# Kernel tuning notes

Hardware: AMD Instinct MI355X
Metric: run time of the kernel (lower is better)

The kernel has to match this reference:

```python
import jax, jax.numpy as jnp
import numpy as np

WINDOW_SIZE = 11
SIGMA = 1.5
C1 = 0.01 ** 2
C2 = 0.03 ** 2
MSE_WEIGHT = 1.0
SSIM_WEIGHT = 0.01


def _gaussian_window(channels):
    # 1D gaussian, normalized, then outer product -> [C,1,K,K] depthwise kernel
    coords = np.arange(WINDOW_SIZE) - WINDOW_SIZE // 2
    g = np.exp(-(coords ** 2) / (2.0 * SIGMA ** 2))
    g = g / g.sum()
    w2d = np.outer(g, g).astype(np.float32)  # [K,K]
    w = np.tile(w2d[None, None], (channels, 1, 1, 1))  # [C,1,K,K]
    return jnp.asarray(w)


def _depthwise_conv(x, w):
    # x: [B,C,H,W], w: [C,1,K,K]; SAME padding, groups=C (matches torch conv2d pad=K//2, groups=C)
    pad = WINDOW_SIZE // 2
    return jax.lax.conv_general_dilated(
        x, w,
        window_strides=(1, 1),
        padding=[(pad, pad), (pad, pad)],
        dimension_numbers=('NCHW', 'OIHW', 'NCHW'),
        feature_group_count=x.shape[1],
    )


def setup_inputs() -> dict:
    key = jax.random.key(0)
    k1, k2 = jax.random.split(key)
    shape = (32, 3, 512, 512)
    predicted = jax.random.uniform(k1, shape, dtype=jnp.float32)
    target = jax.random.uniform(k2, shape, dtype=jnp.float32)
    return {"predicted": predicted, "target": target}


def reference(predicted, target):
    # MSE part
    mse_l = jnp.mean((predicted - target) ** 2)

    # SSIM part (standard pytorch-ssim: gaussian window, size_average=True)
    C = predicted.shape[1]
    w = _gaussian_window(C)

    mu1 = _depthwise_conv(predicted, w)
    mu2 = _depthwise_conv(target, w)
    mu1_sq = mu1 * mu1
    mu2_sq = mu2 * mu2
    mu1_mu2 = mu1 * mu2

    sigma1_sq = _depthwise_conv(predicted * predicted, w) - mu1_sq
    sigma2_sq = _depthwise_conv(target * target, w) - mu2_sq
    sigma12 = _depthwise_conv(predicted * target, w) - mu1_mu2

    ssim_map = ((2.0 * mu1_mu2 + C1) * (2.0 * sigma12 + C2)) / (
        (mu1_sq + mu2_sq + C1) * (sigma1_sq + sigma2_sq + C2)
    )
    ssim_val = jnp.mean(ssim_map)

    return MSE_WEIGHT * mse_l + SSIM_WEIGHT * (1.0 - ssim_val)
```

## Files before the change

kernel.cpp:

```cpp
#include <hip/hip_runtime.h>
#include <hip/hip_fp16.h>


#define WSZ   512
#define TW    64
#define TH    32
#define HALO  5
#define IN_H  (TH + 2*HALO)
#define NPOS  32
#define GX    (WSZ / TW)
#define GY    (WSZ / TH)
#define NSLOT 64
#define SSIM_C1 0.0001f
#define SSIM_C2 0.0009f

#define W0 0.00102838f
#define W1 0.00759876f
#define W2 0.03600080f
#define W3 0.10936080f
#define W4 0.21300560f
#define W5 0.26601170f

static __device__ __forceinline__ __half2 pk(float a, float b) {
    return __builtin_bit_cast(__half2, __builtin_amdgcn_cvt_pkrtz(a, b));
}
static __device__ __forceinline__ __half2 stagger(__half2 hi, __half2 lo) {
    return __builtin_bit_cast(__half2,
        __builtin_amdgcn_alignbit(__builtin_bit_cast(unsigned, hi),
                                  __builtin_bit_cast(unsigned, lo), 16));
}

__launch_bounds__(256, 6)
__global__ void fused_mse_ssim(const float* __restrict__ P,
                               const float* __restrict__ T,
                               float* __restrict__ ws) {
    __shared__ float4 sAB[IN_H][NPOS];
    __shared__ float  red[2][4];

    const int tid = threadIdx.x;
    const int gx0 = blockIdx.x * TW;
    const int gy0 = blockIdx.y * TH;
    const size_t plane = (size_t)blockIdx.z * (WSZ * (size_t)WSZ);
    const float* Pp = P + plane;
    const float* Tp = T + plane;

    const float gwf[11] = {W0,W1,W2,W3,W4,W5,W4,W3,W2,W1,W0};
    unsigned gwh[11];
    #pragma unroll
    for (int k = 0; k < 11; ++k)
        gwh[k] = __builtin_amdgcn_readfirstlane(
                     __builtin_bit_cast(unsigned, __float2half2_rn(gwf[k])));

    float mse = 0.f;

    const bool interior = (blockIdx.x != 0) && (blockIdx.x != GX - 1) &&
                          (blockIdx.y != 0) && (blockIdx.y != GY - 1);

    for (int it = tid; it < IN_H * 8; it += 256) {
        const int r  = it >> 3;
        const int q  = it & 7;
        const int gy = gy0 - HALO + r;
        const int cb = gx0 + q * 8 - 8;
        const float* prow = Pp + ((long)gy * WSZ + cb);
        const float* trow = Tp + ((long)gy * WSZ + cb);
        const bool mrow = ((unsigned)(r - HALO) < (unsigned)TH);

        __half2 As[12], Ad[12];

        if (interior) {
            #pragma unroll
            for (int b = 0; b < 6; ++b) {
                const float4 pv = *(const float4*)(prow + 4 * b);
                const float4 tv = *(const float4*)(trow + 4 * b);
                const float s0 = pv.x + tv.x, s1 = pv.y + tv.y;
                const float s2 = pv.z + tv.z, s3 = pv.w + tv.w;
                const float d0 = pv.x - tv.x, d1 = pv.y - tv.y;
                const float d2 = pv.z - tv.z, d3 = pv.w - tv.w;
                As[2*b]   = pk(s0, s1); As[2*b+1] = pk(s2, s3);
                Ad[2*b]   = pk(d0, d1); Ad[2*b+1] = pk(d2, d3);
                if ((b == 2 || b == 3) && mrow) {
                    mse = fmaf(d0, d0, mse); mse = fmaf(d1, d1, mse);
                    mse = fmaf(d2, d2, mse); mse = fmaf(d3, d3, mse);
                }
            }
        } else {
            const bool rv = ((unsigned)gy < (unsigned)WSZ);
            #pragma unroll
            for (int b = 0; b < 6; ++b) {
                const unsigned c = (unsigned)(cb + 4 * b);
                float4 pv = make_float4(0.f, 0.f, 0.f, 0.f);
                float4 tv = make_float4(0.f, 0.f, 0.f, 0.f);
                if (rv && c < (unsigned)WSZ) {
                    pv = *(const float4*)(prow + 4 * b);
                    tv = *(const float4*)(trow + 4 * b);
                }
                const float s0 = pv.x + tv.x, s1 = pv.y + tv.y;
                const float s2 = pv.z + tv.z, s3 = pv.w + tv.w;
                const float d0 = pv.x - tv.x, d1 = pv.y - tv.y;
                const float d2 = pv.z - tv.z, d3 = pv.w - tv.w;
                As[2*b]   = pk(s0, s1); As[2*b+1] = pk(s2, s3);
                Ad[2*b]   = pk(d0, d1); Ad[2*b+1] = pk(d2, d3);
                if ((b == 2 || b == 3) && mrow) {
                    mse = fmaf(d0, d0, mse); mse = fmaf(d1, d1, mse);
                    mse = fmaf(d2, d2, mse); mse = fmaf(d3, d3, mse);
                }
            }
        }

        const __half2 z = __float2half2_rn(0.f);
        __half2 aS[4]  = {z, z, z, z};
        __half2 aD[4]  = {z, z, z, z};
        __half2 aSS[4] = {z, z, z, z};
        __half2 aDD[4] = {z, z, z, z};

        #pragma unroll
        for (int jj = 0; jj <= 16; ++jj) {
            const int j = jj + 3;
            __half2 vs, vd;
            if (j & 1) {
                vs = stagger(As[(j >> 1) + 1], As[j >> 1]);
                vd = stagger(Ad[(j >> 1) + 1], Ad[j >> 1]);
            } else {
                vs = As[j >> 1];
                vd = Ad[j >> 1];
            }
            const __half2 vss = __hmul2(vs, vs);
            const __half2 vdd = __hmul2(vd, vd);
            #pragma unroll
            for (int m = 0; m < 4; ++m) {
                const int k = jj - 2 * m;
                if (k >= 0 && k < 11) {
                    const __half2 w = __builtin_bit_cast(__half2, gwh[k]);
                    aS[m]  = __hfma2(w, vs,  aS[m]);
                    aD[m]  = __hfma2(w, vd,  aD[m]);
                    aSS[m] = __hfma2(w, vss, aSS[m]);
                    aDD[m] = __hfma2(w, vdd, aDD[m]);
                }
            }
        }

        #pragma unroll
        for (int m = 0; m < 4; ++m)
            sAB[r][8 * m + q] = make_float4(
                __builtin_bit_cast(float, aS[m]),  __builtin_bit_cast(float, aD[m]),
                __builtin_bit_cast(float, aSS[m]), __builtin_bit_cast(float, aDD[m]));
    }
    __syncthreads();

    const int q2  = tid & 31;
    const int col = ((q2 & 3) << 3) | (q2 >> 2);
    const int y0  = (tid >> 5) << 2;

    const __half2 z2 = __float2half2_rn(0.f);
    __half2 acc[4][4];
    #pragma unroll
    for (int a = 0; a < 4; ++a) {
        acc[a][0] = z2; acc[a][1] = z2; acc[a][2] = z2; acc[a][3] = z2;
    }

    #pragma unroll
    for (int j = 0; j < 14; ++j) {
        const float4 ab = sAB[y0 + j][col];
        const __half2 hS  = __builtin_bit_cast(__half2, ab.x);
        const __half2 hD  = __builtin_bit_cast(__half2, ab.y);
        const __half2 hSS = __builtin_bit_cast(__half2, ab.z);
        const __half2 hDD = __builtin_bit_cast(__half2, ab.w);
        #pragma unroll
        for (int a = 0; a < 4; ++a) {
            const int k = j - a;
            if (k >= 0 && k < 11) {
                const __half2 w = __builtin_bit_cast(__half2, gwh[k]);
                acc[a][0] = __hfma2(w, hS,  acc[a][0]);
                acc[a][1] = __hfma2(w, hD,  acc[a][1]);
                acc[a][2] = __hfma2(w, hSS, acc[a][2]);
                acc[a][3] = __hfma2(w, hDD, acc[a][3]);
            }
        }
    }

    float ssim = 0.f;
    #pragma unroll
    for (int a = 0; a < 4; ++a) {
        const float2 Av = __half22float2(acc[a][0]);
        const float2 Bv = __half22float2(acc[a][1]);
        const float2 Xv = __half22float2(acc[a][2]);
        const float2 Yv = __half22float2(acc[a][3]);
        #pragma unroll
        for (int e = 0; e < 2; ++e) {
            const float A = e ? Av.y : Av.x;
            const float B = e ? Bv.y : Bv.x;
            const float X = e ? Xv.y : Xv.x;
            const float Y = e ? Yv.y : Yv.x;
            const float a2 = A * A;
            const float b2 = B * B;
            const float P1 = a2 + b2;
            const float M1 = a2 - b2;
            const float num1 = fmaf(0.5f, M1, SSIM_C1);
            const float den1 = fmaf(0.5f, P1, SSIM_C1);
            const float num2 = fmaf(0.5f, (X - Y) - M1, SSIM_C2);
            const float den2 = fmaf(0.5f, (X + Y) - P1, SSIM_C2);
            ssim = fmaf(num1 * num2, __builtin_amdgcn_rcpf(den1 * den2), ssim);
        }
    }

    #pragma unroll
    for (int off = 32; off > 0; off >>= 1) {
        mse  += __shfl_down(mse, off);
        ssim += __shfl_down(ssim, off);
    }
    const int wid = tid >> 6;
    if ((tid & 63) == 0) { red[0][wid] = mse; red[1][wid] = ssim; }
    __syncthreads();
    if (tid == 0) {
        const float m = red[0][0] + red[0][1] + red[0][2] + red[0][3];
        const float s = red[1][0] + red[1][1] + red[1][2] + red[1][3];
        const int bid  = (blockIdx.z * gridDim.y + blockIdx.y) * gridDim.x + blockIdx.x;
        const int slot = (bid & (NSLOT - 1)) * 16;
        atomicAdd(&ws[slot + 0], m);
        atomicAdd(&ws[slot + 1], s);
    }
}

__global__ void finalize_loss(const float* __restrict__ ws,
                              float* __restrict__ out, float invN) {
    const int t = threadIdx.x;
    float m = ws[t * 16 + 0];
    float s = ws[t * 16 + 1];
    #pragma unroll
    for (int off = 32; off > 0; off >>= 1) {
        m += __shfl_down(m, off);
        s += __shfl_down(s, off);
    }
    if (t == 0) out[0] = m * invN + 0.01f * (1.f - s * invN);
}

extern "C" void kernel_launch(void* const* d_in, const int* in_sizes, int n_in,
                              void* d_out, int out_size, void* d_ws, size_t ws_size,
                              hipStream_t stream) {
    const float* P = (const float*)d_in[0];
    const float* T = (const float*)d_in[1];
    float* out = (float*)d_out;
    float* ws  = (float*)d_ws;

    const int planes = in_sizes[0] / (WSZ * WSZ);
    const float invN = 1.f / (float)in_sizes[0];

    (void)hipMemsetAsync(ws, 0, NSLOT * 16 * sizeof(float), stream);
    dim3 grid(GX, GY, planes);
    fused_mse_ssim<<<grid, 256, 0, stream>>>(P, T, ws);
    finalize_loss<<<1, 64, 0, stream>>>(ws, out, invN);
}
```

Baseline: 234.3 us.

## Stream row chunks through a ring buffer per block and fuse finalize via last-block reduction

Each block now covers a 64x256 strip and walks it in 32-row chunks, keeping horizontally blurred rows in a 48-row circular shared buffer. Only the first chunk loads the 10-row halo, so redundant halo loads and the horizontal pass on them are removed. The separate finalize kernel is replaced by a last-block-done atomic counter that performs the final reduction inside the main kernel, saving a launch. The cost is a smaller grid with fewer, longer blocks, which lowers parallelism and latency hiding, plus an extra barrier per chunk.

```diff
diff --git a/kernel.cpp b/kernel.cpp
--- a/kernel.cpp
+++ b/kernel.cpp
@@ -4,12 +4,13 @@
 
 #define WSZ   512
 #define TW    64
-#define TH    32
+#define GX    (WSZ / TW)
+#define HH    256
+#define CH    32
+#define NCH   (HH / CH)
+#define BUF   48
+#define NPOS  32
 #define HALO  5
-#define IN_H  (TH + 2*HALO)
-#define NPOS  32
-#define GX    (WSZ / TW)
-#define GY    (WSZ / TH)
 #define NSLOT 64
 #define SSIM_C1 0.0001f
 #define SSIM_C2 0.0009f
@@ -33,16 +34,20 @@
 __launch_bounds__(256, 6)
 __global__ void fused_mse_ssim(const float* __restrict__ P,
                                const float* __restrict__ T,
-                               float* __restrict__ ws) {
-    __shared__ float4 sAB[IN_H][NPOS];
+                               float* __restrict__ ws,
+                               float* __restrict__ out,
+                               float invN, int nblocks) {
+    __shared__ float4 sAB[BUF][NPOS];
     __shared__ float  red[2][4];
+    __shared__ int    sLast;
 
     const int tid = threadIdx.x;
     const int gx0 = blockIdx.x * TW;
-    const int gy0 = blockIdx.y * TH;
+    const int gyb = blockIdx.y * HH;
     const size_t plane = (size_t)blockIdx.z * (WSZ * (size_t)WSZ);
     const float* Pp = P + plane;
     const float* Tp = T + plane;
+    const bool xedge = (blockIdx.x == 0) || (blockIdx.x == GX - 1);
 
     const float gwf[11] = {W0,W1,W2,W3,W4,W5,W4,W3,W2,W1,W0};
     unsigned gwh[11];
@@ -52,155 +57,168 @@
                      __builtin_bit_cast(unsigned, __float2half2_rn(gwf[k])));
 
     float mse = 0.f;
-
-    const bool interior = (blockIdx.x != 0) && (blockIdx.x != GX - 1) &&
-                          (blockIdx.y != 0) && (blockIdx.y != GY - 1);
-
-    for (int it = tid; it < IN_H * 8; it += 256) {
-        const int r  = it >> 3;
-        const int q  = it & 7;
-        const int gy = gy0 - HALO + r;
-        const int cb = gx0 + q * 8 - 8;
-        const float* prow = Pp + ((long)gy * WSZ + cb);
-        const float* trow = Tp + ((long)gy * WSZ + cb);
-        const bool mrow = ((unsigned)(r - HALO) < (unsigned)TH);
-
-        __half2 As[12], Ad[12];
-
-        if (interior) {
-            #pragma unroll
-            for (int b = 0; b < 6; ++b) {
-                const float4 pv = *(const float4*)(prow + 4 * b);
-                const float4 tv = *(const float4*)(trow + 4 * b);
-                const float s0 = pv.x + tv.x, s1 = pv.y + tv.y;
-                const float s2 = pv.z + tv.z, s3 = pv.w + tv.w;
-                const float d0 = pv.x - tv.x, d1 = pv.y - tv.y;
-                const float d2 = pv.z - tv.z, d3 = pv.w - tv.w;
-                As[2*b]   = pk(s0, s1); As[2*b+1] = pk(s2, s3);
-                Ad[2*b]   = pk(d0, d1); Ad[2*b+1] = pk(d2, d3);
-                if ((b == 2 || b == 3) && mrow) {
-                    mse = fmaf(d0, d0, mse); mse = fmaf(d1, d1, mse);
-                    mse = fmaf(d2, d2, mse); mse = fmaf(d3, d3, mse);
-                }
-            }
-        } else {
-            const bool rv = ((unsigned)gy < (unsigned)WSZ);
-            #pragma unroll
-            for (int b = 0; b < 6; ++b) {
-                const unsigned c = (unsigned)(cb + 4 * b);
-                float4 pv = make_float4(0.f, 0.f, 0.f, 0.f);
-                float4 tv = make_float4(0.f, 0.f, 0.f, 0.f);
-                if (rv && c < (unsigned)WSZ) {
-                    pv = *(const float4*)(prow + 4 * b);
-                    tv = *(const float4*)(trow + 4 * b);
-                }
-                const float s0 = pv.x + tv.x, s1 = pv.y + tv.y;
-                const float s2 = pv.z + tv.z, s3 = pv.w + tv.w;
-                const float d0 = pv.x - tv.x, d1 = pv.y - tv.y;
-                const float d2 = pv.z - tv.z, d3 = pv.w - tv.w;
-                As[2*b]   = pk(s0, s1); As[2*b+1] = pk(s2, s3);
-                Ad[2*b]   = pk(d0, d1); Ad[2*b+1] = pk(d2, d3);
-                if ((b == 2 || b == 3) && mrow) {
-                    mse = fmaf(d0, d0, mse); mse = fmaf(d1, d1, mse);
-                    mse = fmaf(d2, d2, mse); mse = fmaf(d3, d3, mse);
-                }
-            }
+    float ssim = 0.f;
+
+    for (int c = 0; c < NCH; ++c) {
+        const int nIt = (c == 0) ? 42 * 8 : 32 * 8;
+        const int lrb = (c == 0) ? 0 : c * CH + 2 * HALO;
+        for (int it = tid; it < nIt; it += 256) {
+            const int r    = it >> 3;
+            const int q    = it & 7;
+            const int lr   = lrb + r;
+            const int gy   = gyb + lr - HALO;
+            const int slot = lr % BUF;
+            const bool rv   = ((unsigned)gy < (unsigned)WSZ);
+            const bool mrow = ((unsigned)(lr - HALO) < (unsigned)HH);
+            const int cb = gx0 + q * 8 - 8;
+            const float* prow = Pp + ((long)gy * WSZ + cb);
+            const float* trow = Tp + ((long)gy * WSZ + cb);
+
+            const __half2 z = __float2half2_rn(0.f);
+            __half2 As[12], Ad[12];
+
+            if (!xedge) {
+                if (rv) {
+                    #pragma unroll
+                    for (int b = 0; b < 6; ++b) {
+                        const float4 pv = *(const float4*)(prow + 4 * b);
+                        const float4 tv = *(const float4*)(trow + 4 * b);
+                        const float s0 = pv.x + tv.x, s1 = pv.y + tv.y;
+                        const float s2 = pv.z + tv.z, s3 = pv.w + tv.w;
+                        const float d0 = pv.x - tv.x, d1 = pv.y - tv.y;
+                        const float d2 = pv.z - tv.z, d3 = pv.w - tv.w;
+                        As[2*b]   = pk(s0, s1); As[2*b+1] = pk(s2, s3);
+                        Ad[2*b]   = pk(d0, d1); Ad[2*b+1] = pk(d2, d3);
+                        if ((b == 2 || b == 3) && mrow) {
+                            mse = fmaf(d0, d0, mse); mse = fmaf(d1, d1, mse);
+                            mse = fmaf(d2, d2, mse); mse = fmaf(d3, d3, mse);
+                        }
+                    }
+                } else {
+                    #pragma unroll
+                    for (int b = 0; b < 12; ++b) { As[b] = z; Ad[b] = z; }
+                }
+            } else {
+                #pragma unroll
+                for (int b = 0; b < 6; ++b) {
+                    const unsigned cc = (unsigned)(cb + 4 * b);
+                    float4 pv = make_float4(0.f, 0.f, 0.f, 0.f);
+                    float4 tv = make_float4(0.f, 0.f, 0.f, 0.f);
+                    if (rv && cc < (unsigned)WSZ) {
+                        pv = *(const float4*)(prow + 4 * b);
+                        tv = *(const float4*)(trow + 4 * b);
+                    }
+                    const float s0 = pv.x + tv.x, s1 = pv.y + tv.y;
+                    const float s2 = pv.z + tv.z, s3 = pv.w + tv.w;
+                    const float d0 = pv.x - tv.x, d1 = pv.y - tv.y;
+                    const float d2 = pv.z - tv.z, d3 = pv.w - tv.w;
+                    As[2*b]   = pk(s0, s1); As[2*b+1] = pk(s2, s3);
+                    Ad[2*b]   = pk(d0, d1); Ad[2*b+1] = pk(d2, d3);
+                    if ((b == 2 || b == 3) && mrow) {
+                        mse = fmaf(d0, d0, mse); mse = fmaf(d1, d1, mse);
+                        mse = fmaf(d2, d2, mse); mse = fmaf(d3, d3, mse);
+                    }
+                }
+            }
+
+            __half2 aS[4]  = {z, z, z, z};
+            __half2 aD[4]  = {z, z, z, z};
+            __half2 aSS[4] = {z, z, z, z};
+            __half2 aDD[4] = {z, z, z, z};
+
+            #pragma unroll
+            for (int jj = 0; jj <= 16; ++jj) {
+                const int j = jj + 3;
+                __half2 vs, vd;
+                if (j & 1) {
+                    vs = stagger(As[(j >> 1) + 1], As[j >> 1]);
+                    vd = stagger(Ad[(j >> 1) + 1], Ad[j >> 1]);
+                } else {
+                    vs = As[j >> 1];
+                    vd = Ad[j >> 1];
+                }
+                const __half2 vss = __hmul2(vs, vs);
+                const __half2 vdd = __hmul2(vd, vd);
+                #pragma unroll
+                for (int m = 0; m < 4; ++m) {
+                    const int k = jj - 2 * m;
+                    if (k >= 0 && k < 11) {
+                        const __half2 w = __builtin_bit_cast(__half2, gwh[k]);
+                        aS[m]  = __hfma2(w, vs,  aS[m]);
+                        aD[m]  = __hfma2(w, vd,  aD[m]);
+                        aSS[m] = __hfma2(w, vss, aSS[m]);
+                        aDD[m] = __hfma2(w, vdd, aDD[m]);
+                    }
+                }
+            }
+
+            #pragma unroll
+            for (int m = 0; m < 4; ++m)
+                sAB[slot][8 * m + q] = make_float4(
+                    __builtin_bit_cast(float, aS[m]),  __builtin_bit_cast(float, aD[m]),
+                    __builtin_bit_cast(float, aSS[m]), __builtin_bit_cast(float, aDD[m]));
         }
-
-        const __half2 z = __float2half2_rn(0.f);
-        __half2 aS[4]  = {z, z, z, z};
-        __half2 aD[4]  = {z, z, z, z};
-        __half2 aSS[4] = {z, z, z, z};
-        __half2 aDD[4] = {z, z, z, z};
-
-        #pragma unroll
-        for (int jj = 0; jj <= 16; ++jj) {
-            const int j = jj + 3;
-            __half2 vs, vd;
-            if (j & 1) {
-                vs = stagger(As[(j >> 1) + 1], As[j >> 1]);
-                vd = stagger(Ad[(j >> 1) + 1], Ad[j >> 1]);
-            } else {
-                vs = As[j >> 1];
-                vd = Ad[j >> 1];
-            }
-            const __half2 vss = __hmul2(vs, vs);
-            const __half2 vdd = __hmul2(vd, vd);
-            #pragma unroll
-            for (int m = 0; m < 4; ++m) {
-                const int k = jj - 2 * m;
-                if (k >= 0 && k < 11) {
-                    const __half2 w = __builtin_bit_cast(__half2, gwh[k]);
-                    aS[m]  = __hfma2(w, vs,  aS[m]);
-                    aD[m]  = __hfma2(w, vd,  aD[m]);
-                    aSS[m] = __hfma2(w, vss, aSS[m]);
-                    aDD[m] = __hfma2(w, vdd, aDD[m]);
+        __syncthreads();
+
+        {
+            const int q2  = tid & 31;
+            const int col = ((q2 & 3) << 3) | (q2 >> 2);
+            const int y0l = c * CH + ((tid >> 5) << 2);
+            const int s0  = y0l % BUF;
+
+            const __half2 z2 = __float2half2_rn(0.f);
+            __half2 acc[4][4];
+            #pragma unroll
+            for (int a = 0; a < 4; ++a) {
+                acc[a][0] = z2; acc[a][1] = z2; acc[a][2] = z2; acc[a][3] = z2;
+            }
+
+            #pragma unroll
+            for (int j = 0; j < 14; ++j) {
+                int s = s0 + j; if (s >= BUF) s -= BUF;
+                const float4 ab = sAB[s][col];
+                const __half2 hS  = __builtin_bit_cast(__half2, ab.x);
+                const __half2 hD  = __builtin_bit_cast(__half2, ab.y);
+                const __half2 hSS = __builtin_bit_cast(__half2, ab.z);
+                const __half2 hDD = __builtin_bit_cast(__half2, ab.w);
+                #pragma unroll
+                for (int a = 0; a < 4; ++a) {
+                    const int k = j - a;
+                    if (k >= 0 && k < 11) {
+                        const __half2 w = __builtin_bit_cast(__half2, gwh[k]);
+                        acc[a][0] = __hfma2(w, hS,  acc[a][0]);
+                        acc[a][1] = __hfma2(w, hD,  acc[a][1]);
+                        acc[a][2] = __hfma2(w, hSS, acc[a][2]);
+                        acc[a][3] = __hfma2(w, hDD, acc[a][3]);
+                    }
+                }
+            }
+
+            #pragma unroll
+            for (int a = 0; a < 4; ++a) {
+                const float2 Av = __half22float2(acc[a][0]);
+                const float2 Bv = __half22float2(acc[a][1]);
+                const float2 Xv = __half22float2(acc[a][2]);
+                const float2 Yv = __half22float2(acc[a][3]);
+                #pragma unroll
+                for (int e = 0; e < 2; ++e) {
+                    const float A = e ? Av.y : Av.x;
+                    const float B = e ? Bv.y : Bv.x;
+                    const float X = e ? Xv.y : Xv.x;
+                    const float Y = e ? Yv.y : Yv.x;
+                    const float a2 = A * A;
+                    const float b2 = B * B;
+                    const float P1 = a2 + b2;
+                    const float M1 = a2 - b2;
+                    const float num1 = fmaf(0.5f, M1, SSIM_C1);
+                    const float den1 = fmaf(0.5f, P1, SSIM_C1);
+                    const float num2 = fmaf(0.5f, (X - Y) - M1, SSIM_C2);
+                    const float den2 = fmaf(0.5f, (X + Y) - P1, SSIM_C2);
+                    ssim = fmaf(num1 * num2, __builtin_amdgcn_rcpf(den1 * den2), ssim);
                 }
             }
         }
-
-        #pragma unroll
-        for (int m = 0; m < 4; ++m)
-            sAB[r][8 * m + q] = make_float4(
-                __builtin_bit_cast(float, aS[m]),  __builtin_bit_cast(float, aD[m]),
-                __builtin_bit_cast(float, aSS[m]), __builtin_bit_cast(float, aDD[m]));
-    }
-    __syncthreads();
-
-    const int q2  = tid & 31;
-    const int col = ((q2 & 3) << 3) | (q2 >> 2);
-    const int y0  = (tid >> 5) << 2;
-
-    const __half2 z2 = __float2half2_rn(0.f);
-    __half2 acc[4][4];
-    #pragma unroll
-    for (int a = 0; a < 4; ++a) {
-        acc[a][0] = z2; acc[a][1] = z2; acc[a][2] = z2; acc[a][3] = z2;
-    }
-
-    #pragma unroll
-    for (int j = 0; j < 14; ++j) {
-        const float4 ab = sAB[y0 + j][col];
-        const __half2 hS  = __builtin_bit_cast(__half2, ab.x);
-        const __half2 hD  = __builtin_bit_cast(__half2, ab.y);
-        const __half2 hSS = __builtin_bit_cast(__half2, ab.z);
-        const __half2 hDD = __builtin_bit_cast(__half2, ab.w);
-        #pragma unroll
-        for (int a = 0; a < 4; ++a) {
-            const int k = j - a;
-            if (k >= 0 && k < 11) {
-                const __half2 w = __builtin_bit_cast(__half2, gwh[k]);
-                acc[a][0] = __hfma2(w, hS,  acc[a][0]);
-                acc[a][1] = __hfma2(w, hD,  acc[a][1]);
-                acc[a][2] = __hfma2(w, hSS, acc[a][2]);
-                acc[a][3] = __hfma2(w, hDD, acc[a][3]);
-            }
-        }
-    }
-
-    float ssim = 0.f;
-    #pragma unroll
-    for (int a = 0; a < 4; ++a) {
-        const float2 Av = __half22float2(acc[a][0]);
-        const float2 Bv = __half22float2(acc[a][1]);
-        const float2 Xv = __half22float2(acc[a][2]);
-        const float2 Yv = __half22float2(acc[a][3]);
-        #pragma unroll
-        for (int e = 0; e < 2; ++e) {
-            const float A = e ? Av.y : Av.x;
-            const float B = e ? Bv.y : Bv.x;
-            const float X = e ? Xv.y : Xv.x;
-            const float Y = e ? Yv.y : Yv.x;
-            const float a2 = A * A;
-            const float b2 = B * B;
-            const float P1 = a2 + b2;
-            const float M1 = a2 - b2;
-            const float num1 = fmaf(0.5f, M1, SSIM_C1);
-            const float den1 = fmaf(0.5f, P1, SSIM_C1);
-            const float num2 = fmaf(0.5f, (X - Y) - M1, SSIM_C2);
-            const float den2 = fmaf(0.5f, (X + Y) - P1, SSIM_C2);
-            ssim = fmaf(num1 * num2, __builtin_amdgcn_rcpf(den1 * den2), ssim);
-        }
+        __syncthreads();
     }
 
     #pragma unroll
@@ -218,20 +236,25 @@
         const int slot = (bid & (NSLOT - 1)) * 16;
         atomicAdd(&ws[slot + 0], m);
         atomicAdd(&ws[slot + 1], s);
-    }
-}
-
-__global__ void finalize_loss(const float* __restrict__ ws,
-                              float* __restrict__ out, float invN) {
-    const int t = threadIdx.x;
-    float m = ws[t * 16 + 0];
-    float s = ws[t * 16 + 1];
-    #pragma unroll
-    for (int off = 32; off > 0; off >>= 1) {
-        m += __shfl_down(m, off);
-        s += __shfl_down(s, off);
-    }
-    if (t == 0) out[0] = m * invN + 0.01f * (1.f - s * invN);
+        __threadfence();
+        const unsigned old = __hip_atomic_fetch_add(
+            (unsigned*)(ws + NSLOT * 16), 1u,
+            __ATOMIC_ACQ_REL, __HIP_MEMORY_SCOPE_AGENT);
+        sLast = (old == (unsigned)(nblocks - 1)) ? 1 : 0;
+    }
+    __syncthreads();
+    if (sLast && tid < 64) {
+        float m = __hip_atomic_load(&ws[tid * 16 + 0], __ATOMIC_ACQUIRE,
+                                    __HIP_MEMORY_SCOPE_AGENT);
+        float s = __hip_atomic_load(&ws[tid * 16 + 1], __ATOMIC_ACQUIRE,
+                                    __HIP_MEMORY_SCOPE_AGENT);
+        #pragma unroll
+        for (int off = 32; off > 0; off >>= 1) {
+            m += __shfl_down(m, off);
+            s += __shfl_down(s, off);
+        }
+        if (tid == 0) out[0] = m * invN + 0.01f * (1.f - s * invN);
+    }
 }
 
 extern "C" void kernel_launch(void* const* d_in, const int* in_sizes, int n_in,
@@ -242,11 +265,11 @@
     float* out = (float*)d_out;
     float* ws  = (float*)d_ws;
 
-    const int planes = in_sizes[0] / (WSZ * WSZ);
-    const float invN = 1.f / (float)in_sizes[0];
-
-    (void)hipMemsetAsync(ws, 0, NSLOT * 16 * sizeof(float), stream);
-    dim3 grid(GX, GY, planes);
-    fused_mse_ssim<<<grid, 256, 0, stream>>>(P, T, ws);
-    finalize_loss<<<1, 64, 0, stream>>>(ws, out, invN);
-}
+    const int planes  = in_sizes[0] / (WSZ * WSZ);
+    const float invN  = 1.f / (float)in_sizes[0];
+    const int nblocks = GX * 2 * planes;
+
+    (void)hipMemsetAsync(ws, 0, (NSLOT * 16 + 16) * sizeof(float), stream);
+    dim3 grid(GX, 2, planes);
+    fused_mse_ssim<<<grid, 256, 0, stream>>>(P, T, ws, out, invN, nblocks);
+}
```

Measured after the change: 374.8 us. 60.0% more time.

## Use taller 64x64 tiles with 640 threads and swizzled shared layout

Applied to the files above, without the earlier changes.

Doubles tile height to 64 rows so the 10-row halo is amortized over more output rows, which cuts redundant horizontal-pass work and global reads. The block grows to 640 threads so each thread handles exactly one horizontal-pass row segment; 512 of them then run the vertical pass and 128 sit idle. The shared-memory column index is rotated by row to spread LDS bank accesses, and edge handling now keys on the x edge only, with row validity checked per thread. The larger block and the 8-blocks-per-CU launch bound raise register pressure and leave some threads idle.

```diff
diff --git a/kernel.cpp b/kernel.cpp
--- a/kernel.cpp
+++ b/kernel.cpp
@@ -4,12 +4,12 @@
 
 #define WSZ   512
 #define TW    64
-#define TH    32
+#define TH    64
 #define HALO  5
 #define IN_H  (TH + 2*HALO)
-#define NPOS  32
 #define GX    (WSZ / TW)
 #define GY    (WSZ / TH)
+#define NTHR  640
 #define NSLOT 64
 #define SSIM_C1 0.0001f
 #define SSIM_C2 0.0009f
@@ -30,12 +30,12 @@
                                   __builtin_bit_cast(unsigned, lo), 16));
 }
 
-__launch_bounds__(256, 6)
+__launch_bounds__(NTHR, 8)
 __global__ void fused_mse_ssim(const float* __restrict__ P,
                                const float* __restrict__ T,
                                float* __restrict__ ws) {
-    __shared__ float4 sAB[IN_H][NPOS];
-    __shared__ float  red[2][4];
+    __shared__ float4 sAB[IN_H][32];
+    __shared__ float  red[2][NTHR / 64];
 
     const int tid = threadIdx.x;
     const int gx0 = blockIdx.x * TW;
@@ -43,6 +43,7 @@
     const size_t plane = (size_t)blockIdx.z * (WSZ * (size_t)WSZ);
     const float* Pp = P + plane;
     const float* Tp = T + plane;
+    const bool xedge = (blockIdx.x == 0) || (blockIdx.x == GX - 1);
 
     const float gwf[11] = {W0,W1,W2,W3,W4,W5,W4,W3,W2,W1,W0};
     unsigned gwh[11];
@@ -53,25 +54,50 @@
 
     float mse = 0.f;
 
-    const bool interior = (blockIdx.x != 0) && (blockIdx.x != GX - 1) &&
-                          (blockIdx.y != 0) && (blockIdx.y != GY - 1);
-
-    for (int it = tid; it < IN_H * 8; it += 256) {
-        const int r  = it >> 3;
-        const int q  = it & 7;
+    if (tid < IN_H * 8) {
+        const int r  = tid >> 3;
+        const int g  = tid & 7;
         const int gy = gy0 - HALO + r;
-        const int cb = gx0 + q * 8 - 8;
+        const int cb = gx0 + g * 8 - 8;
         const float* prow = Pp + ((long)gy * WSZ + cb);
         const float* trow = Tp + ((long)gy * WSZ + cb);
+        const bool rv   = ((unsigned)gy < (unsigned)WSZ);
         const bool mrow = ((unsigned)(r - HALO) < (unsigned)TH);
 
+        const __half2 z = __float2half2_rn(0.f);
         __half2 As[12], Ad[12];
 
-        if (interior) {
+        if (!xedge) {
+            if (rv) {
+                #pragma unroll
+                for (int b = 0; b < 6; ++b) {
+                    const float4 pv = *(const float4*)(prow + 4 * b);
+                    const float4 tv = *(const float4*)(trow + 4 * b);
+                    const float s0 = pv.x + tv.x, s1 = pv.y + tv.y;
+                    const float s2 = pv.z + tv.z, s3 = pv.w + tv.w;
+                    const float d0 = pv.x - tv.x, d1 = pv.y - tv.y;
+                    const float d2 = pv.z - tv.z, d3 = pv.w - tv.w;
+                    As[2*b]   = pk(s0, s1); As[2*b+1] = pk(s2, s3);
+                    Ad[2*b]   = pk(d0, d1); Ad[2*b+1] = pk(d2, d3);
+                    if ((b == 2 || b == 3) && mrow) {
+                        mse = fmaf(d0, d0, mse); mse = fmaf(d1, d1, mse);
+                        mse = fmaf(d2, d2, mse); mse = fmaf(d3, d3, mse);
+                    }
+                }
+            } else {
+                #pragma unroll
+                for (int b = 0; b < 12; ++b) { As[b] = z; Ad[b] = z; }
+            }
+        } else {
             #pragma unroll
             for (int b = 0; b < 6; ++b) {
-                const float4 pv = *(const float4*)(prow + 4 * b);
-                const float4 tv = *(const float4*)(trow + 4 * b);
+                const unsigned cc = (unsigned)(cb + 4 * b);
+                float4 pv = make_float4(0.f, 0.f, 0.f, 0.f);
+                float4 tv = make_float4(0.f, 0.f, 0.f, 0.f);
+                if (rv && cc < (unsigned)WSZ) {
+                    pv = *(const float4*)(prow + 4 * b);
+                    tv = *(const float4*)(trow + 4 * b);
+                }
                 const float s0 = pv.x + tv.x, s1 = pv.y + tv.y;
                 const float s2 = pv.z + tv.z, s3 = pv.w + tv.w;
                 const float d0 = pv.x - tv.x, d1 = pv.y - tv.y;
@@ -83,31 +109,8 @@
                     mse = fmaf(d2, d2, mse); mse = fmaf(d3, d3, mse);
                 }
             }
-        } else {
-            const bool rv = ((unsigned)gy < (unsigned)WSZ);
-            #pragma unroll
-            for (int b = 0; b < 6; ++b) {
-                const unsigned c = (unsigned)(cb + 4 * b);
-                float4 pv = make_float4(0.f, 0.f, 0.f, 0.f);
-                float4 tv = make_float4(0.f, 0.f, 0.f, 0.f);
-                if (rv && c < (unsigned)WSZ) {
-                    pv = *(const float4*)(prow + 4 * b);
-                    tv = *(const float4*)(trow + 4 * b);
-                }
-                const float s0 = pv.x + tv.x, s1 = pv.y + tv.y;
-                const float s2 = pv.z + tv.z, s3 = pv.w + tv.w;
-                const float d0 = pv.x - tv.x, d1 = pv.y - tv.y;
-                const float d2 = pv.z - tv.z, d3 = pv.w - tv.w;
-                As[2*b]   = pk(s0, s1); As[2*b+1] = pk(s2, s3);
-                Ad[2*b]   = pk(d0, d1); Ad[2*b+1] = pk(d2, d3);
-                if ((b == 2 || b == 3) && mrow) {
-                    mse = fmaf(d0, d0, mse); mse = fmaf(d1, d1, mse);
-                    mse = fmaf(d2, d2, mse); mse = fmaf(d3, d3, mse);
-                }
-            }
-        }
-
-        const __half2 z = __float2half2_rn(0.f);
+        }
+
         __half2 aS[4]  = {z, z, z, z};
         __half2 aD[4]  = {z, z, z, z};
         __half2 aSS[4] = {z, z, z, z};
@@ -141,65 +144,68 @@
 
         #pragma unroll
         for (int m = 0; m < 4; ++m)
-            sAB[r][8 * m + q] = make_float4(
+            sAB[r][(4 * g + m + r) & 31] = make_float4(
                 __builtin_bit_cast(float, aS[m]),  __builtin_bit_cast(float, aD[m]),
                 __builtin_bit_cast(float, aSS[m]), __builtin_bit_cast(float, aDD[m]));
     }
     __syncthreads();
 
-    const int q2  = tid & 31;
-    const int col = ((q2 & 3) << 3) | (q2 >> 2);
-    const int y0  = (tid >> 5) << 2;
-
-    const __half2 z2 = __float2half2_rn(0.f);
-    __half2 acc[4][4];
-    #pragma unroll
-    for (int a = 0; a < 4; ++a) {
-        acc[a][0] = z2; acc[a][1] = z2; acc[a][2] = z2; acc[a][3] = z2;
-    }
-
-    #pragma unroll
-    for (int j = 0; j < 14; ++j) {
-        const float4 ab = sAB[y0 + j][col];
-        const __half2 hS  = __builtin_bit_cast(__half2, ab.x);
-        const __half2 hD  = __builtin_bit_cast(__half2, ab.y);
-        const __half2 hSS = __builtin_bit_cast(__half2, ab.z);
-        const __half2 hDD = __builtin_bit_cast(__half2, ab.w);
+    float ssim = 0.f;
+
+    if (tid < 512) {
+        const int q2 = tid & 31;
+        const int y0 = (tid >> 5) << 2;
+
+        const __half2 z2 = __float2half2_rn(0.f);
+        __half2 acc[4][4];
         #pragma unroll
         for (int a = 0; a < 4; ++a) {
-            const int k = j - a;
-            if (k >= 0 && k < 11) {
-                const __half2 w = __builtin_bit_cast(__half2, gwh[k]);
-                acc[a][0] = __hfma2(w, hS,  acc[a][0]);
-                acc[a][1] = __hfma2(w, hD,  acc[a][1]);
-                acc[a][2] = __hfma2(w, hSS, acc[a][2]);
-                acc[a][3] = __hfma2(w, hDD, acc[a][3]);
-            }
-        }
-    }
-
-    float ssim = 0.f;
-    #pragma unroll
-    for (int a = 0; a < 4; ++a) {
-        const float2 Av = __half22float2(acc[a][0]);
-        const float2 Bv = __half22float2(acc[a][1]);
-        const float2 Xv = __half22float2(acc[a][2]);
-        const float2 Yv = __half22float2(acc[a][3]);
-        #pragma unroll
-        for (int e = 0; e < 2; ++e) {
-            const float A = e ? Av.y : Av.x;
-            const float B = e ? Bv.y : Bv.x;
-            const float X = e ? Xv.y : Xv.x;
-            const float Y = e ? Yv.y : Yv.x;
-            const float a2 = A * A;
-            const float b2 = B * B;
-            const float P1 = a2 + b2;
-            const float M1 = a2 - b2;
-            const float num1 = fmaf(0.5f, M1, SSIM_C1);
-            const float den1 = fmaf(0.5f, P1, SSIM_C1);
-            const float num2 = fmaf(0.5f, (X - Y) - M1, SSIM_C2);
-            const float den2 = fmaf(0.5f, (X + Y) - P1, SSIM_C2);
-            ssim = fmaf(num1 * num2, __builtin_amdgcn_rcpf(den1 * den2), ssim);
+            acc[a][0] = z2; acc[a][1] = z2; acc[a][2] = z2; acc[a][3] = z2;
+        }
+
+        #pragma unroll
+        for (int j = 0; j < 14; ++j) {
+            const int lr = y0 + j;
+            const float4 ab = sAB[lr][(q2 + lr) & 31];
+            const __half2 hS  = __builtin_bit_cast(__half2, ab.x);
+            const __half2 hD  = __builtin_bit_cast(__half2, ab.y);
+            const __half2 hSS = __builtin_bit_cast(__half2, ab.z);
+            const __half2 hDD = __builtin_bit_cast(__half2, ab.w);
+            #pragma unroll
+            for (int a = 0; a < 4; ++a) {
+                const int k = j - a;
+                if (k >= 0 && k < 11) {
+                    const __half2 w = __builtin_bit_cast(__half2, gwh[k]);
+                    acc[a][0] = __hfma2(w, hS,  acc[a][0]);
+                    acc[a][1] = __hfma2(w, hD,  acc[a][1]);
+                    acc[a][2] = __hfma2(w, hSS, acc[a][2]);
+                    acc[a][3] = __hfma2(w, hDD, acc[a][3]);
+                }
+            }
+        }
+
+        #pragma unroll
+        for (int a = 0; a < 4; ++a) {
+            const float2 Av = __half22float2(acc[a][0]);
+            const float2 Bv = __half22float2(acc[a][1]);
+            const float2 Xv = __half22float2(acc[a][2]);
+            const float2 Yv = __half22float2(acc[a][3]);
+            #pragma unroll
+            for (int e = 0; e < 2; ++e) {
+                const float A = e ? Av.y : Av.x;
+                const float B = e ? Bv.y : Bv.x;
+                const float X = e ? Xv.y : Xv.x;
+                const float Y = e ? Yv.y : Yv.x;
+                const float a2 = A * A;
+                const float b2 = B * B;
+                const float P1 = a2 + b2;
+                const float M1 = a2 - b2;
+                const float num1 = fmaf(0.5f, M1, SSIM_C1);
+                const float den1 = fmaf(0.5f, P1, SSIM_C1);
+                const float num2 = fmaf(0.5f, (X - Y) - M1, SSIM_C2);
+                const float den2 = fmaf(0.5f, (X + Y) - P1, SSIM_C2);
+                ssim = fmaf(num1 * num2, __builtin_amdgcn_rcpf(den1 * den2), ssim);
+            }
         }
     }
 
@@ -212,8 +218,9 @@
     if ((tid & 63) == 0) { red[0][wid] = mse; red[1][wid] = ssim; }
     __syncthreads();
     if (tid == 0) {
-        const float m = red[0][0] + red[0][1] + red[0][2] + red[0][3];
-        const float s = red[1][0] + red[1][1] + red[1][2] + red[1][3];
+        float m = 0.f, s = 0.f;
+        #pragma unroll
+        for (int w = 0; w < NTHR / 64; ++w) { m += red[0][w]; s += red[1][w]; }
         const int bid  = (blockIdx.z * gridDim.y + blockIdx.y) * gridDim.x + blockIdx.x;
         const int slot = (bid & (NSLOT - 1)) * 16;
         atomicAdd(&ws[slot + 0], m);
@@ -247,6 +254,6 @@
 
     (void)hipMemsetAsync(ws, 0, NSLOT * 16 * sizeof(float), stream);
     dim3 grid(GX, GY, planes);
-    fused_mse_ssim<<<grid, 256, 0, stream>>>(P, T, ws);
+    fused_mse_ssim<<<grid, NTHR, 0, stream>>>(P, T, ws);
     finalize_loss<<<1, 64, 0, stream>>>(ws, out, invN);
 }
```

Result: no change. 237.7 us (+1.5%).
